# Kernel optimization log

Hardware: AMD Instinct MI355X
Metric: run time of the kernel (lower is better)

The kernel has to match this reference:

```python
import jax, jax.numpy as jnp
import numpy as np

N = 100000        # nodes
E = 1600000       # edges (avg degree 16)
IN_DIM = 128
OUT_DIM = 64
HEADS = 4
SLOPE = 0.2
CLIP_LO, CLIP_HI = 0.005, 10.0


def setup_inputs() -> dict:
    key = jax.random.key(0)
    k1, k2, k3, k4 = jax.random.split(key, 4)
    h = jax.random.normal(k1, (N, IN_DIM), dtype=jnp.float32)
    edges = jax.random.randint(k2, (2, E), 0, N, dtype=jnp.int64)
    # per-head Linear(in_dim, out_dim, bias=False) weights, applied as h @ W[k]
    W = jax.random.normal(k3, (HEADS, IN_DIM, OUT_DIM), dtype=jnp.float32) / np.sqrt(IN_DIM)
    # per-head Linear(2*out_dim, 1, bias=False) attention vectors
    a = jax.random.normal(k4, (HEADS, 2 * OUT_DIM), dtype=jnp.float32) / np.sqrt(2 * OUT_DIM)
    return {"h": h, "edges": edges, "W": W, "a": a}


def reference(h, edges, W, a):
    src, dst = edges[0], edges[1]
    outs = []
    for k in range(HEADS):  # small fixed loop over structurally distinct heads
        hw = h @ W[k]                                   # [N, OUT]
        # a(concat(hw[src], hw[dst])) == (hw @ a1)[src] + (hw @ a2)[dst]
        s_src = hw @ a[k, :OUT_DIM]                     # [N]
        s_dst = hw @ a[k, OUT_DIM:]                     # [N]
        logit = s_src[src] + s_dst[dst]                 # [E]
        e = jnp.clip(jnp.exp(jax.nn.leaky_relu(logit, SLOPE)), CLIP_LO, CLIP_HI)
        denom = jax.ops.segment_sum(e, dst, num_segments=N)   # per-dst softmax denom
        alpha = e / denom[dst]                          # [E]
        msg = hw[src] * alpha[:, None]                  # [E, OUT]
        outs.append(jax.ops.segment_sum(msg, dst, num_segments=N))
    # concatenate=False -> mean over heads
    return jnp.stack(outs, axis=-1).mean(axis=-1)
```

## Files before the change

### kernel.cpp

```cpp
#include <hip/hip_runtime.h>
#include <hip/hip_fp16.h>

#define N_NODES 100000
#define N_EDGES 1600000
#define IN_DIM  128
#define OUT_DIM 64
#define HEADS   4
#define SLOPE   0.2f
#define CLIP_LO 0.005f
#define CLIP_HI 10.0f
#define NRANGE 250
#define RANGE_SZ 400
#define EDGES_PER_BLK 2048
#define CHUNKS 782
#define GEMM_BLOCKS 1563
#define S_BLOCKS 391
#define BUCKET 48
#define BIN_CAP 32

typedef short bf16x8 __attribute__((ext_vector_type(8)));
typedef float f32x4  __attribute__((ext_vector_type(4)));

__device__ __forceinline__ short f2bf(float x) {
    union { float f; unsigned u; } v; v.f = x;
    unsigned r = (v.u + 0x7FFF + ((v.u >> 16) & 1)) >> 16;
    return (short)r;
}
__device__ __forceinline__ unsigned short f2hbits(float x) {
    union { __half h; unsigned short u; } c; c.h = __float2half(x); return c.u;
}
__device__ __forceinline__ float hbits2f(unsigned short b) {
    union { __half h; unsigned short u; } c; c.u = b; return __half2float(c.h);
}

__global__ __launch_bounds__(256) void prep_kernel(const float* __restrict__ W,
                                                   const float* __restrict__ a,
                                                   short* __restrict__ WcatT,
                                                   float* __restrict__ Wa) {
    int idx = blockIdx.x * 256 + threadIdx.x;
    if (idx < 256 * 128) {
        int n = idx >> 7, i = idx & 127;
        int k = n >> 6, j = n & 63;
        WcatT[idx] = f2bf(W[((size_t)k * IN_DIM + i) * OUT_DIM + j]);
    } else if (idx < 256 * 128 + 1024) {
        int o = idx - 256 * 128;
        int k = o >> 8, half = (o >> 7) & 1, i = o & 127;
        const float* wrow = W + ((size_t)k * IN_DIM + i) * OUT_DIM;
        const float* av   = a + k * 2 * OUT_DIM + half * OUT_DIM;
        float acc = 0.f;
#pragma unroll 8
        for (int j = 0; j < OUT_DIM; ++j) acc += wrow[j] * av[j];
        Wa[o] = acc;
    }
}

__global__ __launch_bounds__(256) void s_bin(const float* __restrict__ h,
                                             const float* __restrict__ Wa,
                                             const int* __restrict__ edges,
                                             unsigned* __restrict__ bins,
                                             int* __restrict__ binCnt,
                                             float* __restrict__ sS,
                                             float* __restrict__ sD) {
    __shared__ __align__(16) char smem[33024];
    if (blockIdx.x >= S_BLOCKS) {
        int* bcnt = (int*)smem;
        unsigned* bents = (unsigned*)(smem + 1024);
        const int c = blockIdx.x - S_BLOCKS;
        const int base = c * EDGES_PER_BLK + threadIdx.x * 8;
        for (int t = threadIdx.x; t < NRANGE; t += 256) bcnt[t] = 0;
        __syncthreads();
        if (base < N_EDGES) {
            int4 s0 = *(const int4*)(edges + base);
            int4 s1 = *(const int4*)(edges + base + 4);
            int4 d0 = *(const int4*)(edges + N_EDGES + base);
            int4 d1 = *(const int4*)(edges + N_EDGES + base + 4);
            int ss[8] = {s0.x, s0.y, s0.z, s0.w, s1.x, s1.y, s1.z, s1.w};
            int dd[8] = {d0.x, d0.y, d0.z, d0.w, d1.x, d1.y, d1.z, d1.w};
#pragma unroll
            for (int u = 0; u < 8; ++u) {
                unsigned d = (unsigned)dd[u];
                unsigned r = d / (unsigned)RANGE_SZ;
                int pos = atomicAdd(&bcnt[r], 1);
                if (pos < BIN_CAP)
                    bents[r * BIN_CAP + pos] = ((unsigned)ss[u] << 9) | (d - r * RANGE_SZ);
            }
        }
        __syncthreads();
        for (int idx = threadIdx.x; idx < NRANGE * BIN_CAP; idx += 256) {
            int r = idx >> 5, i = idx & 31;
            int n = bcnt[r]; if (n > BIN_CAP) n = BIN_CAP;
            if (i < n) bins[((size_t)r * CHUNKS + c) * BIN_CAP + i] = bents[r * BIN_CAP + i];
            if (i == 0) binCnt[r * CHUNKS + c] = n;
        }
        return;
    }

    float* wa_s = (float*)smem;
    for (int t = threadIdx.x; t < HEADS * 2 * IN_DIM; t += 256) wa_s[t] = Wa[t];
    __syncthreads();
    int n = blockIdx.x * 256 + threadIdx.x;
    if (n >= N_NODES) return;
    const float4* hv = (const float4*)(h + (size_t)n * IN_DIM);
    const float4* wv = (const float4*)wa_s;
    float acc[8] = {0.f,0.f,0.f,0.f,0.f,0.f,0.f,0.f};
    for (int i4 = 0; i4 < IN_DIM / 4; ++i4) {
        float4 hx = hv[i4];
#pragma unroll
        for (int k2 = 0; k2 < 8; ++k2) {
            float4 w = wv[k2 * (IN_DIM / 4) + i4];
            acc[k2] += hx.x * w.x + hx.y * w.y + hx.z * w.z + hx.w * w.w;
        }
    }
    *(float4*)(sS + (size_t)n * 4) = make_float4(acc[0], acc[2], acc[4], acc[6]);
    *(float4*)(sD + (size_t)n * 4) = make_float4(acc[1], acc[3], acc[5], acc[7]);
}

__device__ __forceinline__ float edge_e(float x) {
    x = x > 0.f ? x : SLOPE * x;
    float ev = __expf(x);
    return fminf(fmaxf(ev, CLIP_LO), CLIP_HI);
}

__global__ __launch_bounds__(256) void gemm_scatter(const float* __restrict__ h,
                                                    const short* __restrict__ WcatT,
                                                    const unsigned* __restrict__ bins,
                                                    const int* __restrict__ binCnt,
                                                    const float4* __restrict__ sArrS,
                                                    const float4* __restrict__ sArrD,
                                                    int* __restrict__ cnt,
                                                    uint4* __restrict__ csr,
                                                    unsigned char* __restrict__ hw8,
                                                    float* __restrict__ scaleArr) {
    __shared__ __align__(16) char smem[64 * 136 * 2];

    if (blockIdx.x < NRANGE) {
        int*    cntL = (int*)smem;
        float4* dvL  = (float4*)(smem + 1664);
        int*    bcL  = (int*)(smem + 8064);
        const int r = blockIdx.x;
        for (int t = threadIdx.x; t < RANGE_SZ; t += 256) {
            cntL[t] = 0;
            dvL[t]  = sArrD[r * RANGE_SZ + t];
        }
        for (int t = threadIdx.x; t < CHUNKS; t += 256) bcL[t] = binCnt[r * CHUNKS + t];
        __syncthreads();

        const int TOT = CHUNKS * BIN_CAP;
        for (int slot = threadIdx.x; slot < TOT; slot += 256) {
            int c = slot >> 5, i = slot & 31;
            if (i >= bcL[c]) continue;
            unsigned u = bins[((size_t)r * CHUNKS + c) * BIN_CAP + i];
            int s  = u >> 9;
            int dl = u & 511;
            float4 sv = sArrS[s];
            float4 dv = dvL[dl];
            uint4 rec;
            rec.x = (unsigned)s;
            rec.y = f2hbits(edge_e(sv.x + dv.x)) | ((unsigned)f2hbits(edge_e(sv.y + dv.y)) << 16);
            rec.z = f2hbits(edge_e(sv.z + dv.z)) | ((unsigned)f2hbits(edge_e(sv.w + dv.w)) << 16);
            rec.w = 0;
            int pos = atomicAdd(&cntL[dl], 1);
            if (pos < BUCKET)
                csr[(size_t)(r * RANGE_SZ + dl) * BUCKET + pos] = rec;
        }
        __syncthreads();
        for (int t = threadIdx.x; t < RANGE_SZ; t += 256) {
            int v = cntL[t];
            cnt[r * RANGE_SZ + t] = v > BUCKET ? BUCKET : v;
        }
        return;
    }

    short (*As)[136] = (short(*)[136])smem;
    const int row0 = (blockIdx.x - NRANGE) * 64;
    const int tid  = threadIdx.x;

#pragma unroll
    for (int u = 0; u < 4; ++u) {
        int e = (tid + u * 256) * 8;
        int r = e >> 7, c = e & 127;
        int grow = row0 + r; if (grow >= N_NODES) grow = N_NODES - 1;
        const float* hp = h + (size_t)grow * IN_DIM + c;
        float4 v0 = *(const float4*)hp;
        float4 v1 = *(const float4*)(hp + 4);
        bf16x8 b;
        b[0]=f2bf(v0.x); b[1]=f2bf(v0.y); b[2]=f2bf(v0.z); b[3]=f2bf(v0.w);
        b[4]=f2bf(v1.x); b[5]=f2bf(v1.y); b[6]=f2bf(v1.z); b[7]=f2bf(v1.w);
        *(bf16x8*)&As[r][c] = b;
    }
    __syncthreads();

    const int wv = tid >> 6, lane = tid & 63;
    const int lrow = lane & 15;
    const int lk   = (lane >> 4) * 8;

    bf16x8 bfr[4][4];
#pragma unroll
    for (int nt = 0; nt < 4; ++nt)
#pragma unroll
        for (int ks = 0; ks < 4; ++ks)
            bfr[nt][ks] = *(const bf16x8*)(WcatT + (size_t)(wv * 64 + nt * 16 + lrow) * 128 + ks * 32 + lk);

    f32x4 acc[4][4] = {};
#pragma unroll
    for (int ks = 0; ks < 4; ++ks) {
        bf16x8 afr[4];
#pragma unroll
        for (int mt = 0; mt < 4; ++mt)
            afr[mt] = *(const bf16x8*)&As[mt * 16 + lrow][ks * 32 + lk];
#pragma unroll
        for (int mt = 0; mt < 4; ++mt)
#pragma unroll
            for (int nt = 0; nt < 4; ++nt)
                acc[mt][nt] = __builtin_amdgcn_mfma_f32_16x16x32_bf16(afr[mt], bfr[nt][ks], acc[mt][nt], 0, 0, 0);
    }

    const int rgrp = lane >> 4;
#pragma unroll
    for (int mt = 0; mt < 4; ++mt)
#pragma unroll
        for (int reg = 0; reg < 4; ++reg) {
            int g = row0 + mt * 16 + rgrp * 4 + reg;
            float m = fmaxf(fmaxf(fabsf(acc[mt][0][reg]), fabsf(acc[mt][1][reg])),
                            fmaxf(fabsf(acc[mt][2][reg]), fabsf(acc[mt][3][reg])));
#pragma unroll
            for (int off = 1; off < 16; off <<= 1)
                m = fmaxf(m, __shfl_xor(m, off));
            float scale = m > 0.f ? m * (1.f / 127.f) : 1.f;
            float inv   = m > 0.f ? 127.f / m : 0.f;
            uchar4 q;
            q.x = (unsigned char)(int)rintf(acc[mt][0][reg] * inv + 128.f);
            q.y = (unsigned char)(int)rintf(acc[mt][1][reg] * inv + 128.f);
            q.z = (unsigned char)(int)rintf(acc[mt][2][reg] * inv + 128.f);
            q.w = (unsigned char)(int)rintf(acc[mt][3][reg] * inv + 128.f);
            if (g < N_NODES) {
                *(uchar4*)(hw8 + (size_t)g * 256 + wv * 64 + lrow * 4) = q;
                if (lrow == 0) scaleArr[(size_t)g * 4 + wv] = scale;
            }
        }
}

__device__ __forceinline__ float pickw(const uint4& r, int kh) {
    unsigned wp = (kh & 2) ? r.z : r.y;
    return hbits2f((unsigned short)((kh & 1) ? (wp >> 16) : (wp & 0xffff)));
}
__device__ __forceinline__ void qacc(float4& lo, float4& hi, uint2 g, float ws) {
    float wb = -128.f * ws;
    unsigned x = g.x, y = g.y;
    lo.x += fmaf((float)( x        & 255u), ws, wb);
    lo.y += fmaf((float)((x >> 8 ) & 255u), ws, wb);
    lo.z += fmaf((float)((x >> 16) & 255u), ws, wb);
    lo.w += fmaf((float)( x >> 24        ), ws, wb);
    hi.x += fmaf((float)( y        & 255u), ws, wb);
    hi.y += fmaf((float)((y >> 8 ) & 255u), ws, wb);
    hi.z += fmaf((float)((y >> 16) & 255u), ws, wb);
    hi.w += fmaf((float)( y >> 24        ), ws, wb);
}

__global__ __launch_bounds__(256) void msg_csr(const int* __restrict__ cnt,
                                               const uint4* __restrict__ csr,
                                               const unsigned char* __restrict__ hw8,
                                               const float* __restrict__ scaleArr,
                                               float* __restrict__ out) {
    int wid  = (blockIdx.x * 256 + threadIdx.x) >> 6;
    int lane = threadIdx.x & 63;
    if (wid >= N_NODES) return;
    const size_t start = (size_t)wid * BUCKET;
    int dg = cnt[wid];
    if (dg > BUCKET) dg = BUCKET;

    const int es = lane >> 5;
    const int kh = (lane & 31) >> 3;
    const int cg = lane & 7;
    const size_t coff = (size_t)((kh << 6) + (cg << 3));

    float4 alo = make_float4(0.f,0.f,0.f,0.f), ahi = make_float4(0.f,0.f,0.f,0.f);
    float den = 0.f;
    int i = 0;
    for (; i + 8 <= dg; i += 8) {
        uint4 r0 = csr[start + i     + es];
        uint4 r1 = csr[start + i + 2 + es];
        uint4 r2 = csr[start + i + 4 + es];
        uint4 r3 = csr[start + i + 6 + es];
        uint2 g0 = *(const uint2*)(hw8 + (((size_t)r0.x) << 8) + coff);
        uint2 g1 = *(const uint2*)(hw8 + (((size_t)r1.x) << 8) + coff);
        uint2 g2 = *(const uint2*)(hw8 + (((size_t)r2.x) << 8) + coff);
        uint2 g3 = *(const uint2*)(hw8 + (((size_t)r3.x) << 8) + coff);
        float sc0 = scaleArr[(size_t)r0.x * 4 + kh];
        float sc1 = scaleArr[(size_t)r1.x * 4 + kh];
        float sc2 = scaleArr[(size_t)r2.x * 4 + kh];
        float sc3 = scaleArr[(size_t)r3.x * 4 + kh];
        float w0 = pickw(r0, kh);
        float w1 = pickw(r1, kh);
        float w2 = pickw(r2, kh);
        float w3 = pickw(r3, kh);
        den += (w0 + w1) + (w2 + w3);
        qacc(alo, ahi, g0, w0 * sc0);
        qacc(alo, ahi, g1, w1 * sc1);
        qacc(alo, ahi, g2, w2 * sc2);
        qacc(alo, ahi, g3, w3 * sc3);
    }
    for (; i + 4 <= dg; i += 4) {
        uint4 r0 = csr[start + i     + es];
        uint4 r1 = csr[start + i + 2 + es];
        uint2 g0 = *(const uint2*)(hw8 + (((size_t)r0.x) << 8) + coff);
        uint2 g1 = *(const uint2*)(hw8 + (((size_t)r1.x) << 8) + coff);
        float sc0 = scaleArr[(size_t)r0.x * 4 + kh];
        float sc1 = scaleArr[(size_t)r1.x * 4 + kh];
        float w0 = pickw(r0, kh);
        float w1 = pickw(r1, kh);
        den += w0 + w1;
        qacc(alo, ahi, g0, w0 * sc0);
        qacc(alo, ahi, g1, w1 * sc1);
    }
    for (; i < dg; i += 2) {
        int idx = i + es;
        bool valid = idx < dg;
        if (idx >= dg) idx = dg - 1;
        uint4 r = csr[start + idx];
        uint2 g = *(const uint2*)(hw8 + (((size_t)r.x) << 8) + coff);
        float sc = scaleArr[(size_t)r.x * 4 + kh];
        float w = valid ? pickw(r, kh) : 0.f;
        den += w;
        qacc(alo, ahi, g, w * sc);
    }

    den += __shfl_xor(den, 32);
    float invk = den > 0.f ? 0.25f / den : 0.f;
    alo.x *= invk; alo.y *= invk; alo.z *= invk; alo.w *= invk;
    ahi.x *= invk; ahi.y *= invk; ahi.z *= invk; ahi.w *= invk;

#pragma unroll
    for (int off = 8; off < 64; off <<= 1) {
        alo.x += __shfl_xor(alo.x, off); alo.y += __shfl_xor(alo.y, off);
        alo.z += __shfl_xor(alo.z, off); alo.w += __shfl_xor(alo.w, off);
        ahi.x += __shfl_xor(ahi.x, off); ahi.y += __shfl_xor(ahi.y, off);
        ahi.z += __shfl_xor(ahi.z, off); ahi.w += __shfl_xor(ahi.w, off);
    }
    if (lane < 8) {
        float* op = out + (size_t)wid * OUT_DIM + (cg << 1);
        *(float2*)(op)      = make_float2(alo.x, ahi.x);
        *(float2*)(op + 16) = make_float2(alo.y, ahi.y);
        *(float2*)(op + 32) = make_float2(alo.z, ahi.z);
        *(float2*)(op + 48) = make_float2(alo.w, ahi.w);
    }
}

extern "C" void kernel_launch(void* const* d_in, const int* in_sizes, int n_in,
                              void* d_out, int out_size, void* d_ws, size_t ws_size,
                              hipStream_t stream) {
    const float* h     = (const float*)d_in[0];
    const int*   edges = (const int*)d_in[1];
    const float* W     = (const float*)d_in[2];
    const float* a     = (const float*)d_in[3];
    float* out = (float*)d_out;

    char* ws = (char*)d_ws;
    unsigned char* hw8 = (unsigned char*)(ws);
    float*  scaleArr= (float*) (ws + 25600000);
    float*  sArrS   = (float*) (ws + 27200000);
    float*  sArrD   = (float*) (ws + 28800000);
    short*  WcatT   = (short*) (ws + 30400000);
    float*  Wa      = (float*) (ws + 30465536);
    int*    cnt     = (int*)   (ws + 30469632);
    int*    binCnt  = (int*)   (ws + 30869632);
    uint4*  csr     = (uint4*) (ws + 31651632);

    unsigned* bins = (unsigned*)d_out;

    prep_kernel<<<132, 256, 0, stream>>>(W, a, WcatT, Wa);
    s_bin<<<S_BLOCKS + CHUNKS, 256, 0, stream>>>(h, Wa, edges, bins, binCnt,
                                                 sArrS, sArrD);
    gemm_scatter<<<NRANGE + GEMM_BLOCKS, 256, 0, stream>>>(
        h, WcatT, bins, binCnt, (const float4*)sArrS, (const float4*)sArrD,
        cnt, csr, hw8, scaleArr);

    msg_csr<<<(N_NODES + 3) / 4, 256, 0, stream>>>(cnt, csr, hw8, scaleArr, out);
}
```

Baseline: 199.8 us.

## Compact per-range edge bins into dense arrays via global atomic offsets

Each binning block now reserves a contiguous slot in a per-range dense array through a global atomicAdd, instead of writing fixed-capacity per-chunk bins. The scatter stage then streams a packed list with vectorized uint4 loads and no longer walks every padded slot or reads per-chunk counts. The aim is to cut the mostly empty slot iteration and the binCnt traffic, at the cost of global atomics, an extra memset, and a per-range cap of 8192 that could drop edges if a range overflows.

```diff
diff --git a/kernel.cpp b/kernel.cpp
--- a/kernel.cpp
+++ b/kernel.cpp
@@ -17,6 +17,7 @@
 #define S_BLOCKS 391
 #define BUCKET 48
 #define BIN_CAP 32
+#define CAPR 8192
 
 typedef short bf16x8 __attribute__((ext_vector_type(8)));
 typedef float f32x4  __attribute__((ext_vector_type(4)));
@@ -57,14 +58,15 @@
 __global__ __launch_bounds__(256) void s_bin(const float* __restrict__ h,
                                              const float* __restrict__ Wa,
                                              const int* __restrict__ edges,
-                                             unsigned* __restrict__ bins,
-                                             int* __restrict__ binCnt,
+                                             unsigned* __restrict__ dense,
+                                             int* __restrict__ rangeCnt,
                                              float* __restrict__ sS,
                                              float* __restrict__ sD) {
-    __shared__ __align__(16) char smem[33024];
+    __shared__ __align__(16) char smem[35072];
     if (blockIdx.x >= S_BLOCKS) {
         int* bcnt = (int*)smem;
         unsigned* bents = (unsigned*)(smem + 1024);
+        int* posL = (int*)(smem + 33024);
         const int c = blockIdx.x - S_BLOCKS;
         const int base = c * EDGES_PER_BLK + threadIdx.x * 8;
         for (int t = threadIdx.x; t < NRANGE; t += 256) bcnt[t] = 0;
@@ -86,11 +88,18 @@
             }
         }
         __syncthreads();
+        if (threadIdx.x < NRANGE) {
+            int n = bcnt[threadIdx.x]; if (n > BIN_CAP) n = BIN_CAP;
+            bcnt[threadIdx.x] = n;
+            posL[threadIdx.x] = atomicAdd(&rangeCnt[threadIdx.x], n);
+        }
+        __syncthreads();
         for (int idx = threadIdx.x; idx < NRANGE * BIN_CAP; idx += 256) {
             int r = idx >> 5, i = idx & 31;
-            int n = bcnt[r]; if (n > BIN_CAP) n = BIN_CAP;
-            if (i < n) bins[((size_t)r * CHUNKS + c) * BIN_CAP + i] = bents[r * BIN_CAP + i];
-            if (i == 0) binCnt[r * CHUNKS + c] = n;
+            if (i < bcnt[r]) {
+                int p = posL[r] + i;
+                if (p < CAPR) dense[(size_t)r * CAPR + p] = bents[r * BIN_CAP + i];
+            }
         }
         return;
     }
@@ -123,8 +132,8 @@
 
 __global__ __launch_bounds__(256) void gemm_scatter(const float* __restrict__ h,
                                                     const short* __restrict__ WcatT,
-                                                    const unsigned* __restrict__ bins,
-                                                    const int* __restrict__ binCnt,
+                                                    const unsigned* __restrict__ dense,
+                                                    const int* __restrict__ rangeCnt,
                                                     const float4* __restrict__ sArrS,
                                                     const float4* __restrict__ sArrD,
                                                     int* __restrict__ cnt,
@@ -136,32 +145,42 @@
     if (blockIdx.x < NRANGE) {
         int*    cntL = (int*)smem;
         float4* dvL  = (float4*)(smem + 1664);
-        int*    bcL  = (int*)(smem + 8064);
         const int r = blockIdx.x;
         for (int t = threadIdx.x; t < RANGE_SZ; t += 256) {
             cntL[t] = 0;
             dvL[t]  = sArrD[r * RANGE_SZ + t];
         }
-        for (int t = threadIdx.x; t < CHUNKS; t += 256) bcL[t] = binCnt[r * CHUNKS + t];
         __syncthreads();
 
-        const int TOT = CHUNKS * BIN_CAP;
-        for (int slot = threadIdx.x; slot < TOT; slot += 256) {
-            int c = slot >> 5, i = slot & 31;
-            if (i >= bcL[c]) continue;
-            unsigned u = bins[((size_t)r * CHUNKS + c) * BIN_CAP + i];
-            int s  = u >> 9;
-            int dl = u & 511;
-            float4 sv = sArrS[s];
-            float4 dv = dvL[dl];
-            uint4 rec;
-            rec.x = (unsigned)s;
-            rec.y = f2hbits(edge_e(sv.x + dv.x)) | ((unsigned)f2hbits(edge_e(sv.y + dv.y)) << 16);
-            rec.z = f2hbits(edge_e(sv.z + dv.z)) | ((unsigned)f2hbits(edge_e(sv.w + dv.w)) << 16);
-            rec.w = 0;
-            int pos = atomicAdd(&cntL[dl], 1);
-            if (pos < BUCKET)
-                csr[(size_t)(r * RANGE_SZ + dl) * BUCKET + pos] = rec;
+        int n = rangeCnt[r]; if (n > CAPR) n = CAPR;
+        const unsigned* dl = dense + (size_t)r * CAPR;
+        for (int i0 = threadIdx.x * 4; i0 < n; i0 += 1024) {
+            uint4 e4 = *(const uint4*)(dl + i0);
+            unsigned ent[4] = {e4.x, e4.y, e4.z, e4.w};
+            int nv = n - i0; if (nv > 4) nv = 4;
+            float4 sv[4], dv[4];
+#pragma unroll
+            for (int u = 0; u < 4; ++u) {
+                if (u < nv) {
+                    sv[u] = sArrS[ent[u] >> 9];
+                    dv[u] = dvL[ent[u] & 511];
+                }
+            }
+#pragma unroll
+            for (int u = 0; u < 4; ++u) {
+                if (u < nv) {
+                    int s  = ent[u] >> 9;
+                    int dloc = ent[u] & 511;
+                    uint4 rec;
+                    rec.x = (unsigned)s;
+                    rec.y = f2hbits(edge_e(sv[u].x + dv[u].x)) | ((unsigned)f2hbits(edge_e(sv[u].y + dv[u].y)) << 16);
+                    rec.z = f2hbits(edge_e(sv[u].z + dv[u].z)) | ((unsigned)f2hbits(edge_e(sv[u].w + dv[u].w)) << 16);
+                    rec.w = 0;
+                    int pos = atomicAdd(&cntL[dloc], 1);
+                    if (pos < BUCKET)
+                        csr[(size_t)(r * RANGE_SZ + dloc) * BUCKET + pos] = rec;
+                }
+            }
         }
         __syncthreads();
         for (int t = threadIdx.x; t < RANGE_SZ; t += 256) {
@@ -363,16 +382,18 @@
     short*  WcatT   = (short*) (ws + 30400000);
     float*  Wa      = (float*) (ws + 30465536);
     int*    cnt     = (int*)   (ws + 30469632);
-    int*    binCnt  = (int*)   (ws + 30869632);
-    uint4*  csr     = (uint4*) (ws + 31651632);
-
-    unsigned* bins = (unsigned*)d_out;
+    int*    rangeCnt= (int*)   (ws + 30869632);
+    uint4*  csr     = (uint4*) (ws + 30870656);
+
+    unsigned* dense = (unsigned*)d_out;
+
+    hipMemsetAsync(rangeCnt, 0, NRANGE * sizeof(int), stream);
 
     prep_kernel<<<132, 256, 0, stream>>>(W, a, WcatT, Wa);
-    s_bin<<<S_BLOCKS + CHUNKS, 256, 0, stream>>>(h, Wa, edges, bins, binCnt,
+    s_bin<<<S_BLOCKS + CHUNKS, 256, 0, stream>>>(h, Wa, edges, dense, rangeCnt,
                                                  sArrS, sArrD);
     gemm_scatter<<<NRANGE + GEMM_BLOCKS, 256, 0, stream>>>(
-        h, WcatT, bins, binCnt, (const float4*)sArrS, (const float4*)sArrD,
+        h, WcatT, dense, rangeCnt, (const float4*)sArrS, (const float4*)sArrD,
         cnt, csr, hw8, scaleArr);
 
     msg_csr<<<(N_NODES + 3) / 4, 256, 0, stream>>>(cnt, csr, hw8, scaleArr, out);
```

Result: faster. 173.5 us (median of 3 runs) (-13.1%).
